# Kernel optimization log

Measured on AMD Instinct MI355X. Metric: run time of the kernel, lower is better.

Reference implementation:

```python
import jax, jax.numpy as jnp
import numpy as np

DT = 0.01
DAMP_MIN = 5e-4


def setup_inputs() -> dict:
    key = jax.random.key(0)
    ks = jax.random.split(key, 6)
    B_batch, L, Din, N = 4, 4096, 512, 256
    u = jax.random.normal(ks[0], (B_batch, L, Din), dtype=jnp.float32)
    # parameters, initialized as in the torch module
    A_real = jax.random.normal(ks[1], (N,), dtype=jnp.float32) * 0.1 - DAMP_MIN
    A_imag = jax.random.normal(ks[2], (N,), dtype=jnp.float32)
    B_mat = jax.random.normal(ks[3], (N, Din), dtype=jnp.float32) * 0.02
    C_mat = jax.random.normal(ks[4], (Din, N), dtype=jnp.float32) * 0.02
    D_vec = jax.random.normal(ks[5], (Din,), dtype=jnp.float32)
    return {"u": u, "A_real": A_real, "A_imag": A_imag,
            "B_mat": B_mat, "C_mat": C_mat, "D_vec": D_vec}


def reference(u, A_real, A_imag, B_mat, C_mat, D_vec):
    L = u.shape[1]
    # bilinear (Tustin) discretization of diagonal A
    a_real = -jnp.abs(A_real) - DAMP_MIN
    A = jax.lax.complex(a_real, A_imag)                      # [N]
    denom = 1.0 - (DT * 0.5) * A
    A_bar = (1.0 + (DT * 0.5) * A) / denom                   # [N]
    B_bar = DT * B_mat.astype(jnp.complex64) / denom[:, None]  # [N, Din]
    # convolution kernel via explicit powers: K[n, t] = A_bar[n]^t
    k = jnp.arange(L, dtype=jnp.float32)
    A_pow = A_bar[:, None] ** k[None, :]                     # [N, L]
    # project input into state space: v[b, t, n]
    v = jnp.einsum('bld,nd->bln', u.astype(jnp.complex64), B_bar)
    # FFT convolution, zero-padded to 2L (linear convolution)
    n_fft = 2 * L
    v_f = jnp.fft.fft(v, n=n_fft, axis=1)                    # [B, 2L, N]
    k_f = jnp.fft.fft(A_pow.T, n=n_fft, axis=0)              # [2L, N]
    y = jnp.fft.ifft(v_f * k_f[None, :, :], axis=1)[:, :L, :]  # [B, L, N]
    # output projection + skip path
    y_out = jnp.einsum('bln,dn->bld', y, C_mat.astype(jnp.complex64)).real
    return y_out + u * D_vec
```

## Files before the change

kernel.cpp:

```cpp
#include <hip/hip_runtime.h>

#define L_SEQ 4096
#define DIN   512
#define NST   256

typedef __attribute__((ext_vector_type(8))) short short8;
typedef __attribute__((ext_vector_type(4))) float f32x4;

__device__ inline unsigned short f2bf(float f) {
  unsigned u = __builtin_bit_cast(unsigned, f);
  unsigned r = (u + 0x7FFFu + ((u >> 16) & 1u)) >> 16;
  return (unsigned short)r;
}
__device__ inline float bf2f(unsigned short h) {
  unsigned u = ((unsigned)h) << 16;
  return __builtin_bit_cast(float, u);
}

__global__ __launch_bounds__(256) void prepcvt_kernel(
    const float* __restrict__ U, const float* __restrict__ A_real,
    const float* __restrict__ A_imag, const float* __restrict__ B_mat,
    const float* __restrict__ C_mat, float* __restrict__ abr,
    float* __restrict__ abi, unsigned short* __restrict__ bmbf,
    unsigned short* __restrict__ cbf, unsigned short* __restrict__ Ubf) {
  const int i = blockIdx.x * 256 + threadIdx.x;
  const float4 f0 = reinterpret_cast<const float4*>(U)[i * 2];
  const float4 f1 = reinterpret_cast<const float4*>(U)[i * 2 + 1];
  unsigned short o[8] = {f2bf(f0.x), f2bf(f0.y), f2bf(f0.z), f2bf(f0.w),
                         f2bf(f1.x), f2bf(f1.y), f2bf(f1.z), f2bf(f1.w)};
  *reinterpret_cast<short8*>(&Ubf[(size_t)i * 8]) = *reinterpret_cast<short8*>(o);

  const int n = blockIdx.x;
  if (n < NST) {
    const float ar = -fabsf(A_real[n]) - 5e-4f;
    const float ai = A_imag[n];
    const float dr = 1.0f - 0.005f * ar;
    const float di = -0.005f * ai;
    const float inv = 1.0f / (dr * dr + di * di);
    if (threadIdx.x == 0) {
      const float nr = 1.0f + 0.005f * ar;
      const float ni = 0.005f * ai;
      abr[n] = (nr * dr + ni * di) * inv;
      abi[n] = (ni * dr - nr * di) * inv;
    }
    const float cr = 0.01f * dr * inv;
    const float ci = -0.01f * di * inv;
    for (int d = threadIdx.x; d < DIN; d += blockDim.x) {
      const float bv = B_mat[n * DIN + d];
      bmbf[n * DIN + d]         = f2bf(bv * cr);
      bmbf[(NST + n) * DIN + d] = f2bf(bv * ci);
    }
    const size_t cbase = (size_t)(2 * n) * NST;
    for (int k = threadIdx.x; k < 2 * NST; k += blockDim.x)
      cbf[cbase + k] = f2bf(C_mat[cbase + k]);
  }
}

__global__ __launch_bounds__(256, 2) void gemm1_mfma(
    const unsigned short* __restrict__ Ubf,
    const unsigned short* __restrict__ Bmbf,
    unsigned short* __restrict__ V) {
  __shared__ short At[2][128 * 32];
  __shared__ short Bt[2][128 * 32];
  const int tid  = threadIdx.x;
  const int wave = tid >> 6;
  const int lane = tid & 63;
  const int m0 = blockIdx.x * 128;
  const int j0 = blockIdx.y * 128;

  f32x4 acc[4][4];
#pragma unroll
  for (int i = 0; i < 4; ++i)
#pragma unroll
    for (int j = 0; j < 4; ++j) acc[i][j] = (f32x4)0.f;

  const int wr = wave >> 1, wc = wave & 1;
  const int cl = lane & 15;
  const int kq = lane >> 4;

#define STAGE(buf, k0)                                                          \
  {                                                                             \
    _Pragma("unroll")                                                           \
    for (int q = 0; q < 2; ++q) {                                               \
      const int row = wave * 32 + q * 16 + (lane >> 2);                         \
      const int kb  = lane & 3;                                                 \
      const unsigned short* gA = Ubf  + (size_t)(m0 + row) * 512 + (k0) + kb*8; \
      const unsigned short* gB = Bmbf + (size_t)(j0 + row) * 512 + (k0) + kb*8; \
      short* lA = &At[buf][(wave * 32 + q * 16) * 32];                          \
      short* lB = &Bt[buf][(wave * 32 + q * 16) * 32];                          \
      __builtin_amdgcn_global_load_lds(                                         \
          (const __attribute__((address_space(1))) void*)gA,                    \
          (__attribute__((address_space(3))) void*)lA, 16, 0, 0);               \
      __builtin_amdgcn_global_load_lds(                                         \
          (const __attribute__((address_space(1))) void*)gB,                    \
          (__attribute__((address_space(3))) void*)lB, 16, 0, 0);               \
    }                                                                           \
  }

  STAGE(0, 0)
  for (int s = 0; s < 16; ++s) {
    const int cur = s & 1;
    if (s < 15) STAGE(cur ^ 1, (s + 1) * 32)
    __syncthreads();
    short8 a[4], b[4];
#pragma unroll
    for (int f = 0; f < 4; ++f) {
      a[f] = *reinterpret_cast<const short8*>(&At[cur][(wr * 64 + f * 16 + cl) * 32 + kq * 8]);
      b[f] = *reinterpret_cast<const short8*>(&Bt[cur][(wc * 64 + f * 16 + cl) * 32 + kq * 8]);
    }
#pragma unroll
    for (int fm = 0; fm < 4; ++fm)
#pragma unroll
      for (int fn = 0; fn < 4; ++fn)
        acc[fm][fn] = __builtin_amdgcn_mfma_f32_16x16x32_bf16(a[fm], b[fn], acc[fm][fn], 0, 0, 0);
    __syncthreads();
  }
#undef STAGE

  const int bb    = m0 >> 12;
  const int lbase = (m0 & 4095);
#pragma unroll
  for (int fm = 0; fm < 4; ++fm)
#pragma unroll
    for (int fn = 0; fn < 4; ++fn) {
      const int jj = j0 + wc * 64 + fn * 16 + cl;
      const int ll = lbase + wr * 64 + fm * 16 + kq * 4;
      const f32x4 v = acc[fm][fn];
      unsigned short o[4] = {f2bf(v.x), f2bf(v.y), f2bf(v.z), f2bf(v.w)};
      *reinterpret_cast<ushort4*>(&V[((size_t)bb * 512 + jj) * L_SEQ + ll]) =
          *reinterpret_cast<ushort4*>(o);
    }
}

__global__ __launch_bounds__(256) void scan_kernel(
    const unsigned short* __restrict__ V, const float* __restrict__ abr,
    const float* __restrict__ abi, unsigned short* __restrict__ Y) {
  const int b = blockIdx.x >> 8;
  const int n = blockIdx.x & 255;
  const float ar = abr[n], ai = abi[n];
  const unsigned short* vre = V + ((size_t)b * 512 + n) * L_SEQ;
  const unsigned short* vim = V + ((size_t)b * 512 + NST + n) * L_SEQ;
  const int t = threadIdx.x;
  const int lane = t & 63;
  const int wid  = t >> 6;

  float xr[16], xi[16];
#pragma unroll
  for (int q = 0; q < 2; ++q) {
    const short8 r8 = *reinterpret_cast<const short8*>(&vre[t * 16 + q * 8]);
    const short8 i8 = *reinterpret_cast<const short8*>(&vim[t * 16 + q * 8]);
#pragma unroll
    for (int j = 0; j < 8; ++j) {
      xr[q * 8 + j] = bf2f((unsigned short)r8[j]);
      xi[q * 8 + j] = bf2f((unsigned short)i8[j]);
    }
  }
  float yr = 0.f, yi = 0.f;
#pragma unroll
  for (int i = 0; i < 16; ++i) {
    const float t1 = ar * yr - ai * yi + xr[i];
    yi = ar * yi + ai * yr + xi[i];
    yr = t1;
    xr[i] = yr; xi[i] = yi;
  }
  float fr = ar, fi = ai;
#pragma unroll
  for (int s = 0; s < 4; ++s) { const float t2 = fr * fr - fi * fi; fi = 2.f * fr * fi; fr = t2; }

  float er = yr, ei = yi;
  float Fr = fr, Fi = fi;
  float Fkr[6], Fki[6];
#pragma unroll
  for (int s = 0; s < 6; ++s) {
    Fkr[s] = Fr; Fki[s] = Fi;
    const float pr = __shfl_up(er, 1 << s);
    const float pi = __shfl_up(ei, 1 << s);
    if (lane >= (1 << s)) {
      er += Fr * pr - Fi * pi;
      ei += Fr * pi + Fi * pr;
    }
    const float t2 = Fr * Fr - Fi * Fi; Fi = 2.f * Fr * Fi; Fr = t2;
  }

  __shared__ float twr[4], twi[4];
  if (lane == 63) { twr[wid] = er; twi[wid] = ei; }
  __syncthreads();
  float cwr = 0.f, cwi = 0.f;
  for (int w = 0; w < wid; ++w) {
    const float t2 = Fr * cwr - Fi * cwi + twr[w];
    cwi = Fr * cwi + Fi * cwr + twi[w];
    cwr = t2;
  }
  float sxr = __shfl_up(er, 1);
  float sxi = __shfl_up(ei, 1);
  if (lane == 0) { sxr = 0.f; sxi = 0.f; }
  float plr = 1.f, pli = 0.f;
#pragma unroll
  for (int s = 0; s < 6; ++s) {
    if (lane & (1 << s)) {
      const float t2 = plr * Fkr[s] - pli * Fki[s];
      pli = plr * Fki[s] + pli * Fkr[s];
      plr = t2;
    }
  }
  float cr = sxr + plr * cwr - pli * cwi;
  float ci = sxi + plr * cwi + pli * cwr;

  unsigned short o16[16];
  float gr = cr, gi = ci;
#pragma unroll
  for (int i = 0; i < 16; ++i) {
    const float t1 = ar * gr - ai * gi;
    gi = ar * gi + ai * gr;
    gr = t1;
    o16[i] = f2bf(xr[i] + gr);
  }
  unsigned short* yo = Y + ((size_t)b * NST + n) * L_SEQ + t * 16;
  *reinterpret_cast<short8*>(&yo[0]) = *reinterpret_cast<short8*>(&o16[0]);
  *reinterpret_cast<short8*>(&yo[8]) = *reinterpret_cast<short8*>(&o16[8]);
}

__global__ __launch_bounds__(256) void transp_kernel(
    const unsigned short* __restrict__ Y, unsigned short* __restrict__ Yt) {
  __shared__ unsigned short T[64 * 256];
  const int b  = blockIdx.z;
  const int n0 = blockIdx.y * 64;
  const int l0 = blockIdx.x * 256;
  const int t  = threadIdx.x;
  {
    const int nr = t >> 2;
    const int c4 = t & 3;
    const unsigned short* src = Y + ((size_t)b * NST + n0 + nr) * L_SEQ + l0;
#pragma unroll
    for (int h = 0; h < 8; ++h) {
      const int ch = c4 + h * 4;
      const short8 v = *reinterpret_cast<const short8*>(&src[ch * 8]);
      const int p = ch ^ (nr & 7) ^ ((nr >> 3) & 3);
      *reinterpret_cast<short8*>(&T[nr * 256 + p * 8]) = v;
    }
  }
  __syncthreads();
  {
    const int c = t & 7;
#pragma unroll
    for (int h2 = 0; h2 < 8; ++h2) {
      const int l = h2 * 32 + (t >> 3);
      unsigned short o[8];
#pragma unroll
      for (int j = 0; j < 8; ++j) {
        const int p = (l >> 3) ^ j ^ (c & 3);
        o[j] = T[(c * 8 + j) * 256 + p * 8 + (l & 7)];
      }
      *reinterpret_cast<short8*>(&Yt[((size_t)b * L_SEQ + l0 + l) * NST + n0 + c * 8]) =
          *reinterpret_cast<short8*>(o);
    }
  }
}

__global__ __launch_bounds__(256, 2) void gemm2_mfma(
    const unsigned short* __restrict__ Cbf,
    const unsigned short* __restrict__ Yt,
    const unsigned short* __restrict__ Ubf,
    const float* __restrict__ Dv,
    float* __restrict__ out) {
  __shared__ short At[2][128 * 32];
  __shared__ short Bt[2][128 * 32];
  const int tid  = threadIdx.x;
  const int wave = tid >> 6;
  const int lane = tid & 63;
  const int m0 = blockIdx.x * 128;
  const int d0 = blockIdx.y * 128;

  f32x4 acc[4][4];
#pragma unroll
  for (int i = 0; i < 4; ++i)
#pragma unroll
    for (int j = 0; j < 4; ++j) acc[i][j] = (f32x4)0.f;

  const int wr = wave >> 1, wc = wave & 1;
  const int cl = lane & 15;
  const int kq = lane >> 4;

#define STAGE2(buf, k0)                                                         \
  {                                                                             \
    _Pragma("unroll")                                                           \
    for (int q = 0; q < 2; ++q) {                                               \
      const int row = wave * 32 + q * 16 + (lane >> 2);                         \
      const int kb  = lane & 3;                                                 \
      const unsigned short* gA = Cbf + (size_t)(d0 + row) * 256 + (k0) + kb*8;  \
      const unsigned short* gB = Yt  + (size_t)(m0 + row) * 256 + (k0) + kb*8;  \
      short* lA = &At[buf][(wave * 32 + q * 16) * 32];                          \
      short* lB = &Bt[buf][(wave * 32 + q * 16) * 32];                          \
      __builtin_amdgcn_global_load_lds(                                         \
          (const __attribute__((address_space(1))) void*)gA,                    \
          (__attribute__((address_space(3))) void*)lA, 16, 0, 0);               \
      __builtin_amdgcn_global_load_lds(                                         \
          (const __attribute__((address_space(1))) void*)gB,                    \
          (__attribute__((address_space(3))) void*)lB, 16, 0, 0);               \
    }                                                                           \
  }

  STAGE2(0, 0)
  for (int s = 0; s < 8; ++s) {
    const int cur = s & 1;
    if (s < 7) STAGE2(cur ^ 1, (s + 1) * 32)
    __syncthreads();
    short8 a[4], b[4];
#pragma unroll
    for (int f = 0; f < 4; ++f) {
      a[f] = *reinterpret_cast<const short8*>(&At[cur][(wr * 64 + f * 16 + cl) * 32 + kq * 8]);
      b[f] = *reinterpret_cast<const short8*>(&Bt[cur][(wc * 64 + f * 16 + cl) * 32 + kq * 8]);
    }
#pragma unroll
    for (int fm = 0; fm < 4; ++fm)
#pragma unroll
      for (int fn = 0; fn < 4; ++fn)
        acc[fm][fn] = __builtin_amdgcn_mfma_f32_16x16x32_bf16(a[fm], b[fn], acc[fm][fn], 0, 0, 0);
    __syncthreads();
  }
#undef STAGE2

#pragma unroll
  for (int fm = 0; fm < 4; ++fm) {
    const int dd = d0 + wr * 64 + fm * 16 + kq * 4;
    const f32x4 dvv = *reinterpret_cast<const f32x4*>(&Dv[dd]);
#pragma unroll
    for (int fn = 0; fn < 4; ++fn) {
      const size_t ll = m0 + wc * 64 + fn * 16 + cl;
      const size_t base = ll * 512 + dd;
      const ushort4 ub = *reinterpret_cast<const ushort4*>(&Ubf[base]);
      f32x4 o = acc[fm][fn];
      o.x += bf2f(ub.x) * dvv.x; o.y += bf2f(ub.y) * dvv.y;
      o.z += bf2f(ub.z) * dvv.z; o.w += bf2f(ub.w) * dvv.w;
      *reinterpret_cast<f32x4*>(&out[base]) = o;
    }
  }
}

extern "C" void kernel_launch(void* const* d_in, const int* in_sizes, int n_in,
                              void* d_out, int out_size, void* d_ws, size_t ws_size,
                              hipStream_t stream) {
  const float* u      = (const float*)d_in[0];
  const float* A_real = (const float*)d_in[1];
  const float* A_imag = (const float*)d_in[2];
  const float* B_mat  = (const float*)d_in[3];
  const float* C_mat  = (const float*)d_in[4];
  const float* D_vec  = (const float*)d_in[5];
  float* out = (float*)d_out;

  unsigned short* bmbf = (unsigned short*)d_ws;
  unsigned short* cbf  = bmbf + 512 * 512;
  float* abr = (float*)(cbf + 512 * 256);
  float* abi = abr + 256;
  unsigned short* Ubf = (unsigned short*)(abi + 256);
  unsigned short* V   = Ubf + (size_t)16384 * 512;
  unsigned short* Y   = V + (size_t)4 * 512 * 4096;
  unsigned short* Yt  = Y + (size_t)4 * 256 * 4096;

  hipLaunchKernelGGL(prepcvt_kernel, dim3(4096), dim3(256), 0, stream,
                     u, A_real, A_imag, B_mat, C_mat, abr, abi, bmbf, cbf, Ubf);
  hipLaunchKernelGGL(gemm1_mfma, dim3(128, 4), dim3(256), 0, stream, Ubf, bmbf, V);
  hipLaunchKernelGGL(scan_kernel, dim3(1024), dim3(256), 0, stream, V, abr, abi, Y);
  hipLaunchKernelGGL(transp_kernel, dim3(16, 4, 4), dim3(256), 0, stream, Y, Yt);
  hipLaunchKernelGGL(gemm2_mfma, dim3(128, 4), dim3(256), 0, stream, cbf, Yt, Ubf, D_vec, out);
}
```

Baseline: 59.33 us.

## Fuse fp32-to-bf16 input conversion into first GEMM A-tile staging

```diff
diff --git a/kernel.cpp b/kernel.cpp
--- a/kernel.cpp
+++ b/kernel.cpp
@@ -17,47 +17,37 @@
   return __builtin_bit_cast(float, u);
 }
 
-__global__ __launch_bounds__(256) void prepcvt_kernel(
-    const float* __restrict__ U, const float* __restrict__ A_real,
-    const float* __restrict__ A_imag, const float* __restrict__ B_mat,
-    const float* __restrict__ C_mat, float* __restrict__ abr,
-    float* __restrict__ abi, unsigned short* __restrict__ bmbf,
-    unsigned short* __restrict__ cbf, unsigned short* __restrict__ Ubf) {
-  const int i = blockIdx.x * 256 + threadIdx.x;
-  const float4 f0 = reinterpret_cast<const float4*>(U)[i * 2];
-  const float4 f1 = reinterpret_cast<const float4*>(U)[i * 2 + 1];
-  unsigned short o[8] = {f2bf(f0.x), f2bf(f0.y), f2bf(f0.z), f2bf(f0.w),
-                         f2bf(f1.x), f2bf(f1.y), f2bf(f1.z), f2bf(f1.w)};
-  *reinterpret_cast<short8*>(&Ubf[(size_t)i * 8]) = *reinterpret_cast<short8*>(o);
-
+__global__ __launch_bounds__(256) void prep_kernel(
+    const float* __restrict__ A_real, const float* __restrict__ A_imag,
+    const float* __restrict__ B_mat, const float* __restrict__ C_mat,
+    float* __restrict__ abr, float* __restrict__ abi,
+    unsigned short* __restrict__ bmbf, unsigned short* __restrict__ cbf) {
   const int n = blockIdx.x;
-  if (n < NST) {
-    const float ar = -fabsf(A_real[n]) - 5e-4f;
-    const float ai = A_imag[n];
-    const float dr = 1.0f - 0.005f * ar;
-    const float di = -0.005f * ai;
-    const float inv = 1.0f / (dr * dr + di * di);
-    if (threadIdx.x == 0) {
-      const float nr = 1.0f + 0.005f * ar;
-      const float ni = 0.005f * ai;
-      abr[n] = (nr * dr + ni * di) * inv;
-      abi[n] = (ni * dr - nr * di) * inv;
-    }
-    const float cr = 0.01f * dr * inv;
-    const float ci = -0.01f * di * inv;
-    for (int d = threadIdx.x; d < DIN; d += blockDim.x) {
-      const float bv = B_mat[n * DIN + d];
-      bmbf[n * DIN + d]         = f2bf(bv * cr);
-      bmbf[(NST + n) * DIN + d] = f2bf(bv * ci);
-    }
-    const size_t cbase = (size_t)(2 * n) * NST;
-    for (int k = threadIdx.x; k < 2 * NST; k += blockDim.x)
-      cbf[cbase + k] = f2bf(C_mat[cbase + k]);
-  }
+  const float ar = -fabsf(A_real[n]) - 5e-4f;
+  const float ai = A_imag[n];
+  const float dr = 1.0f - 0.005f * ar;
+  const float di = -0.005f * ai;
+  const float inv = 1.0f / (dr * dr + di * di);
+  if (threadIdx.x == 0) {
+    const float nr = 1.0f + 0.005f * ar;
+    const float ni = 0.005f * ai;
+    abr[n] = (nr * dr + ni * di) * inv;
+    abi[n] = (ni * dr - nr * di) * inv;
+  }
+  const float cr = 0.01f * dr * inv;
+  const float ci = -0.01f * di * inv;
+  for (int d = threadIdx.x; d < DIN; d += blockDim.x) {
+    const float bv = B_mat[n * DIN + d];
+    bmbf[n * DIN + d]         = f2bf(bv * cr);
+    bmbf[(NST + n) * DIN + d] = f2bf(bv * ci);
+  }
+  const size_t cbase = (size_t)(2 * n) * NST;
+  for (int k = threadIdx.x; k < 2 * NST; k += blockDim.x)
+    cbf[cbase + k] = f2bf(C_mat[cbase + k]);
 }
 
 __global__ __launch_bounds__(256, 2) void gemm1_mfma(
-    const unsigned short* __restrict__ Ubf,
+    const float* __restrict__ U,
     const unsigned short* __restrict__ Bmbf,
     unsigned short* __restrict__ V) {
   __shared__ short At[2][128 * 32];
@@ -78,29 +68,52 @@
   const int cl = lane & 15;
   const int kq = lane >> 4;
 
-#define STAGE(buf, k0)                                                          \
+  const int arow = tid >> 1;
+  const int acol = (tid & 1) * 16;
+  const float* gA = U + (size_t)(m0 + arow) * 512 + acol;
+
+  f32x4 areg[4];
+#define LOADA(k0)                                                               \
+  {                                                                             \
+    _Pragma("unroll")                                                           \
+    for (int q = 0; q < 4; ++q)                                                 \
+      areg[q] = *reinterpret_cast<const f32x4*>(gA + (k0) + q * 4);             \
+  }
+#define WRITEA(buf)                                                             \
+  {                                                                             \
+    unsigned short o16[16];                                                     \
+    _Pragma("unroll")                                                           \
+    for (int q = 0; q < 4; ++q) {                                               \
+      o16[q * 4 + 0] = f2bf(areg[q].x); o16[q * 4 + 1] = f2bf(areg[q].y);       \
+      o16[q * 4 + 2] = f2bf(areg[q].z); o16[q * 4 + 3] = f2bf(areg[q].w);       \
+    }                                                                           \
+    short* dst = &At[buf][arow * 32 + acol];                                    \
+    *reinterpret_cast<short8*>(dst)     = *reinterpret_cast<short8*>(&o16[0]);  \
+    *reinterpret_cast<short8*>(dst + 8) = *reinterpret_cast<short8*>(&o16[8]);  \
+  }
+#define STAGEB(buf, k0)                                                         \
   {                                                                             \
     _Pragma("unroll")                                                           \
     for (int q = 0; q < 2; ++q) {                                               \
       const int row = wave * 32 + q * 16 + (lane >> 2);                         \
       const int kb  = lane & 3;                                                 \
-      const unsigned short* gA = Ubf  + (size_t)(m0 + row) * 512 + (k0) + kb*8; \
       const unsigned short* gB = Bmbf + (size_t)(j0 + row) * 512 + (k0) + kb*8; \
-      short* lA = &At[buf][(wave * 32 + q * 16) * 32];                          \
       short* lB = &Bt[buf][(wave * 32 + q * 16) * 32];                          \
-      __builtin_amdgcn_global_load_lds(                                         \
-          (const __attribute__((address_space(1))) void*)gA,                    \
-          (__attribute__((address_space(3))) void*)lA, 16, 0, 0);               \
       __builtin_amdgcn_global_load_lds(                                         \
           (const __attribute__((address_space(1))) void*)gB,                    \
           (__attribute__((address_space(3))) void*)lB, 16, 0, 0);               \
     }                                                                           \
   }
 
-  STAGE(0, 0)
+  LOADA(0)
+  STAGEB(0, 0)
   for (int s = 0; s < 16; ++s) {
     const int cur = s & 1;
-    if (s < 15) STAGE(cur ^ 1, (s + 1) * 32)
+    WRITEA(cur)
+    if (s < 15) {
+      LOADA((s + 1) * 32)
+      STAGEB(cur ^ 1, (s + 1) * 32)
+    }
     __syncthreads();
     short8 a[4], b[4];
 #pragma unroll
@@ -115,7 +128,9 @@
         acc[fm][fn] = __builtin_amdgcn_mfma_f32_16x16x32_bf16(a[fm], b[fn], acc[fm][fn], 0, 0, 0);
     __syncthreads();
   }
-#undef STAGE
+#undef LOADA
+#undef WRITEA
+#undef STAGEB
 
   const int bb    = m0 >> 12;
   const int lbase = (m0 & 4095);
@@ -260,7 +275,7 @@
 __global__ __launch_bounds__(256, 2) void gemm2_mfma(
     const unsigned short* __restrict__ Cbf,
     const unsigned short* __restrict__ Yt,
-    const unsigned short* __restrict__ Ubf,
+    const float* __restrict__ U,
     const float* __restrict__ Dv,
     float* __restrict__ out) {
   __shared__ short At[2][128 * 32];
@@ -328,10 +343,10 @@
     for (int fn = 0; fn < 4; ++fn) {
       const size_t ll = m0 + wc * 64 + fn * 16 + cl;
       const size_t base = ll * 512 + dd;
-      const ushort4 ub = *reinterpret_cast<const ushort4*>(&Ubf[base]);
+      const f32x4 uv = *reinterpret_cast<const f32x4*>(&U[base]);
       f32x4 o = acc[fm][fn];
-      o.x += bf2f(ub.x) * dvv.x; o.y += bf2f(ub.y) * dvv.y;
-      o.z += bf2f(ub.z) * dvv.z; o.w += bf2f(ub.w) * dvv.w;
+      o.x += uv.x * dvv.x; o.y += uv.y * dvv.y;
+      o.z += uv.z * dvv.z; o.w += uv.w * dvv.w;
       *reinterpret_cast<f32x4*>(&out[base]) = o;
     }
   }
@@ -352,15 +367,14 @@
   unsigned short* cbf  = bmbf + 512 * 512;
   float* abr = (float*)(cbf + 512 * 256);
   float* abi = abr + 256;
-  unsigned short* Ubf = (unsigned short*)(abi + 256);
-  unsigned short* V   = Ubf + (size_t)16384 * 512;
+  unsigned short* V   = (unsigned short*)(abi + 256);
   unsigned short* Y   = V + (size_t)4 * 512 * 4096;
   unsigned short* Yt  = Y + (size_t)4 * 256 * 4096;
 
-  hipLaunchKernelGGL(prepcvt_kernel, dim3(4096), dim3(256), 0, stream,
-                     u, A_real, A_imag, B_mat, C_mat, abr, abi, bmbf, cbf, Ubf);
-  hipLaunchKernelGGL(gemm1_mfma, dim3(128, 4), dim3(256), 0, stream, Ubf, bmbf, V);
+  hipLaunchKernelGGL(prep_kernel, dim3(NST), dim3(256), 0, stream,
+                     A_real, A_imag, B_mat, C_mat, abr, abi, bmbf, cbf);
+  hipLaunchKernelGGL(gemm1_mfma, dim3(128, 4), dim3(256), 0, stream, u, bmbf, V);
   hipLaunchKernelGGL(scan_kernel, dim3(1024), dim3(256), 0, stream, V, abr, abi, Y);
   hipLaunchKernelGGL(transp_kernel, dim3(16, 4, 4), dim3(256), 0, stream, Y, Yt);
-  hipLaunchKernelGGL(gemm2_mfma, dim3(128, 4), dim3(256), 0, stream, cbf, Yt, Ubf, D_vec, out);
-}
+  hipLaunchKernelGGL(gemm2_mfma, dim3(128, 4), dim3(256), 0, stream, cbf, Yt, u, D_vec, out);
+}
```

New measurement: 62.19 us. +4.8%, slower.
